# Performance work log

Hardware: AMD Instinct MI355X
Metric: run time of the kernel (lower is better)

The kernel has to match this reference:

```python
import jax, jax.numpy as jnp
import numpy as np

B, C_IN, O, K, L = 32, 64, 128, 9, 4096  # L = order*order (vec_size)


def setup_inputs() -> dict:
    key = jax.random.key(0)
    k1, k2, k3, k4 = jax.random.split(key, 4)
    x = jax.random.normal(k1, (B, C_IN, 1, L), dtype=jnp.float32)
    # precomputed irregular group-index map: each row is a permutation-like
    # index list into the vec_size axis; random in-range indices suffice for
    # a correctness baseline.
    index_matrix = jax.random.randint(k2, (K, L), 0, L, dtype=jnp.int32)
    # params (pre-normalized, matching the in-place .data normalization in
    # the torch forward, which is idempotent on already-normalized values)
    wc = jax.random.normal(k3, (O, 1, K), dtype=jnp.float32)
    weight_coeff = wc / jnp.linalg.norm(wc, axis=-1, keepdims=True)
    ev = jax.random.normal(k4, (1, L), dtype=jnp.float32)
    err_vector = ev / jnp.linalg.norm(ev)
    bias = jnp.zeros((O,), dtype=jnp.float32)
    return {"x": x, "weight_coeff": weight_coeff, "err_vector": err_vector,
            "bias": bias, "index_matrix": index_matrix}


def reference(x, weight_coeff, err_vector, bias, index_matrix):
    # normalization performed every forward call in the original module
    ev = err_vector / jnp.linalg.norm(err_vector)                      # [1, L]
    wc = weight_coeff / jnp.linalg.norm(weight_coeff, axis=-1, keepdims=True)  # [O,1,K]
    # gather neighbors via irregular index map, scale by learned vector
    adj = x[:, :, 0, index_matrix] * ev[None, None, :, :]              # [B, C_in, K, L]
    # contract over input channels i and neighborhood k
    res = jnp.einsum('ojk,bikl->bojl', wc, adj)                        # [B, O, 1, L]
    return res + bias[None, :, None, None]
```

## Files before the change

kernel.cpp:

```cpp
#include <hip/hip_runtime.h>

#define NB 32
#define NC 64
#define NO 128
#define NK 9
#define NL 4096

#define OSPLIT 4
#define OPB (NO / OSPLIT)
#define LTILE 1024
#define NLT (NL / LTILE)

typedef float vfloat4 __attribute__((ext_vector_type(4)));
typedef float vfloat2 __attribute__((ext_vector_type(2)));

__global__ __launch_bounds__(256) void colsum_kernel(
    const float* __restrict__ x, const float* __restrict__ ev,
    const float* __restrict__ wc,
    float* __restrict__ colsum, float* __restrict__ evinv,
    float* __restrict__ wcn_ws)
{
    __shared__ vfloat4 part[4][64];
    __shared__ float red[4];

    const int bid = blockIdx.x;
    const int t = threadIdx.x;

    if (bid == 0) {
        float s = 0.f;
#pragma unroll
        for (int r = 0; r < NL / 256; ++r) {
            float v = ev[r * 256 + t];
            s += v * v;
        }
#pragma unroll
        for (int off = 32; off > 0; off >>= 1) s += __shfl_down(s, off, 64);
        if ((t & 63) == 0) red[t >> 6] = s;
        if (t < NO) {
            float w[NK]; float ss = 0.f;
#pragma unroll
            for (int k = 0; k < NK; ++k) { w[k] = wc[t * NK + k]; ss += w[k] * w[k]; }
            const float inv = rsqrtf(ss);
#pragma unroll
            for (int k = 0; k < NK; ++k) wcn_ws[t * NK + k] = w[k] * inv;
        }
        __syncthreads();
        if (t == 0) evinv[0] = rsqrtf(red[0] + red[1] + red[2] + red[3]);
    }

    const int b  = bid >> 4;
    const int lt = bid & 15;
    const int col = t & 63;
    const int cg  = t >> 6;
    const int l = lt * 256 + col * 4;

    const float* xp = x + (size_t)b * NC * NL + (size_t)cg * 16 * NL + l;
    vfloat4 acc = (vfloat4){0.f, 0.f, 0.f, 0.f};
#pragma unroll
    for (int i = 0; i < 16; ++i) {
        vfloat4 v = __builtin_nontemporal_load(
            reinterpret_cast<const vfloat4*>(xp + (size_t)i * NL));
        acc += v;
    }
    part[cg][col] = acc;
    __syncthreads();
    if (t < 64) {
        vfloat4 s = part[0][t];
#pragma unroll
        for (int g = 1; g < 4; ++g) s += part[g][t];
        *reinterpret_cast<vfloat4*>(colsum + (size_t)b * NL + lt * 256 + t * 4) = s;
    }
}

__global__ __launch_bounds__(256) void gmconv_main_kernel(
    const float* __restrict__ wcn, const float* __restrict__ ev,
    const float* __restrict__ bias, const int* __restrict__ idx,
    const float* __restrict__ colsum, const float* __restrict__ evinv_p,
    float* __restrict__ out)
{
    __shared__ float csS[NL];

    const int bid = blockIdx.x;
    const int og = bid & (OSPLIT - 1);
    const int lt = (bid >> 2) & (NLT - 1);
    const int b  = bid >> 4;
    const int t  = threadIdx.x;

    const float evinv = evinv_p[0];
    const int l0 = lt * LTILE + t * 4;

    const vfloat4 e4 = *reinterpret_cast<const vfloat4*>(ev + l0);
    int4 iv[NK];
#pragma unroll
    for (int k = 0; k < NK; ++k)
        iv[k] = *reinterpret_cast<const int4*>(idx + k * NL + l0);

    const float* __restrict__ csg = colsum + (size_t)b * NL;
#pragma unroll
    for (int r = 0; r < NL / (4 * 256); ++r) {
        const int j = (r * 256 + t) * 4;
        *reinterpret_cast<vfloat4*>(&csS[j]) =
            *reinterpret_cast<const vfloat4*>(csg + j);
    }
    __syncthreads();

    const float ex = e4.x * evinv, ey = e4.y * evinv,
                ez = e4.z * evinv, ew = e4.w * evinv;

    vfloat2 g01[NK], g23[NK];
#pragma unroll
    for (int k = 0; k < NK; ++k) {
        g01[k] = (vfloat2){csS[iv[k].x] * ex, csS[iv[k].y] * ey};
        g23[k] = (vfloat2){csS[iv[k].z] * ez, csS[iv[k].w] * ew};
    }

    const int obase = og * OPB;
    float* op = out + ((size_t)b * NO + obase) * NL + l0;
#pragma unroll
    for (int o = 0; o < OPB; ++o) {
        const float* __restrict__ wr = wcn + (obase + o) * NK;
        vfloat2 a01 = (vfloat2){0.f, 0.f};
        vfloat2 a23 = (vfloat2){0.f, 0.f};
#pragma unroll
        for (int k = 0; k < NK; ++k) {
            const float w = wr[k];
            a01 += w * g01[k];
            a23 += w * g23[k];
        }
        const float bb = bias[obase + o];
        const vfloat4 r = (vfloat4){a01.x + bb, a01.y + bb, a23.x + bb, a23.y + bb};
        __builtin_nontemporal_store(r, reinterpret_cast<vfloat4*>(op));
        op += NL;
    }
}

extern "C" void kernel_launch(void* const* d_in, const int* in_sizes, int n_in,
                              void* d_out, int out_size, void* d_ws, size_t ws_size,
                              hipStream_t stream) {
    const float* x    = (const float*)d_in[0];
    const float* wc   = (const float*)d_in[1];
    const float* ev   = (const float*)d_in[2];
    const float* bias = (const float*)d_in[3];
    const int*   idx  = (const int*)d_in[4];
    float* out = (float*)d_out;

    float* wsf    = (float*)d_ws;
    float* evinv  = wsf;
    float* wcn_ws = wsf + 64;
    float* colsum = wsf + 1344;

    hipLaunchKernelGGL(colsum_kernel, dim3(NB * 16), dim3(256), 0, stream,
                       x, ev, wc, colsum, evinv, wcn_ws);
    hipLaunchKernelGGL(gmconv_main_kernel, dim3(NB * NLT * OSPLIT), dim3(256), 0,
                       stream, wcn_ws, ev, bias, idx, colsum, evinv, out);
}
```

Measured before the change: 22.92 us.

## Fuse colsum and conv kernels with per-batch atomic counter barrier

```diff
diff --git a/kernel.cpp b/kernel.cpp
--- a/kernel.cpp
+++ b/kernel.cpp
@@ -6,6 +6,8 @@
 #define NK 9
 #define NL 4096
 
+#define SLICES 16
+#define SL (NL / SLICES)
 #define OSPLIT 4
 #define OPB (NO / OSPLIT)
 #define LTILE 1024
@@ -14,99 +16,92 @@
 typedef float vfloat4 __attribute__((ext_vector_type(4)));
 typedef float vfloat2 __attribute__((ext_vector_type(2)));
 
-__global__ __launch_bounds__(256) void colsum_kernel(
-    const float* __restrict__ x, const float* __restrict__ ev,
-    const float* __restrict__ wc,
-    float* __restrict__ colsum, float* __restrict__ evinv,
-    float* __restrict__ wcn_ws)
+__global__ __launch_bounds__(256) void gmconv_fused(
+    const float* __restrict__ x, const float* __restrict__ wc,
+    const float* __restrict__ ev, const float* __restrict__ bias,
+    const int* __restrict__ idx, float* __restrict__ colsum,
+    int* __restrict__ cnt, float* __restrict__ out)
 {
     __shared__ vfloat4 part[4][64];
     __shared__ float red[4];
-
-    const int bid = blockIdx.x;
-    const int t = threadIdx.x;
-
-    if (bid == 0) {
-        float s = 0.f;
-#pragma unroll
-        for (int r = 0; r < NL / 256; ++r) {
-            float v = ev[r * 256 + t];
-            s += v * v;
-        }
-#pragma unroll
-        for (int off = 32; off > 0; off >>= 1) s += __shfl_down(s, off, 64);
-        if ((t & 63) == 0) red[t >> 6] = s;
-        if (t < NO) {
-            float w[NK]; float ss = 0.f;
-#pragma unroll
-            for (int k = 0; k < NK; ++k) { w[k] = wc[t * NK + k]; ss += w[k] * w[k]; }
-            const float inv = rsqrtf(ss);
-#pragma unroll
-            for (int k = 0; k < NK; ++k) wcn_ws[t * NK + k] = w[k] * inv;
-        }
-        __syncthreads();
-        if (t == 0) evinv[0] = rsqrtf(red[0] + red[1] + red[2] + red[3]);
-    }
-
-    const int b  = bid >> 4;
-    const int lt = bid & 15;
-    const int col = t & 63;
-    const int cg  = t >> 6;
-    const int l = lt * 256 + col * 4;
-
-    const float* xp = x + (size_t)b * NC * NL + (size_t)cg * 16 * NL + l;
-    vfloat4 acc = (vfloat4){0.f, 0.f, 0.f, 0.f};
-#pragma unroll
-    for (int i = 0; i < 16; ++i) {
-        vfloat4 v = __builtin_nontemporal_load(
-            reinterpret_cast<const vfloat4*>(xp + (size_t)i * NL));
-        acc += v;
-    }
-    part[cg][col] = acc;
-    __syncthreads();
-    if (t < 64) {
-        vfloat4 s = part[0][t];
-#pragma unroll
-        for (int g = 1; g < 4; ++g) s += part[g][t];
-        *reinterpret_cast<vfloat4*>(colsum + (size_t)b * NL + lt * 256 + t * 4) = s;
-    }
-}
-
-__global__ __launch_bounds__(256) void gmconv_main_kernel(
-    const float* __restrict__ wcn, const float* __restrict__ ev,
-    const float* __restrict__ bias, const int* __restrict__ idx,
-    const float* __restrict__ colsum, const float* __restrict__ evinv_p,
-    float* __restrict__ out)
-{
+    __shared__ float invS[OPB];
+    __shared__ vfloat2 cbS[OPB];
     __shared__ float csS[NL];
 
     const int bid = blockIdx.x;
-    const int og = bid & (OSPLIT - 1);
-    const int lt = (bid >> 2) & (NLT - 1);
+    const int j  = bid & (SLICES - 1);
     const int b  = bid >> 4;
+    const int og = j & (OSPLIT - 1);
+    const int lt = j >> 2;
     const int t  = threadIdx.x;
 
-    const float evinv = evinv_p[0];
     const int l0 = lt * LTILE + t * 4;
-
     const vfloat4 e4 = *reinterpret_cast<const vfloat4*>(ev + l0);
     int4 iv[NK];
 #pragma unroll
     for (int k = 0; k < NK; ++k)
         iv[k] = *reinterpret_cast<const int4*>(idx + k * NL + l0);
 
-    const float* __restrict__ csg = colsum + (size_t)b * NL;
+    const int col = t & 63;
+    const int cg  = t >> 6;
+    const float* xp = x + (size_t)b * NC * NL + (size_t)cg * 16 * NL
+                        + j * SL + col * 4;
+    vfloat4 xacc = (vfloat4){0.f, 0.f, 0.f, 0.f};
 #pragma unroll
-    for (int r = 0; r < NL / (4 * 256); ++r) {
-        const int j = (r * 256 + t) * 4;
-        *reinterpret_cast<vfloat4*>(&csS[j]) =
-            *reinterpret_cast<const vfloat4*>(csg + j);
+    for (int i = 0; i < 16; ++i)
+        xacc += __builtin_nontemporal_load(
+            reinterpret_cast<const vfloat4*>(xp + (size_t)i * NL));
+
+    float s = 0.f;
+#pragma unroll
+    for (int r = 0; r < 4; ++r) {
+        vfloat4 v = *reinterpret_cast<const vfloat4*>(ev + (r * 256 + t) * 4);
+        s += v.x * v.x + v.y * v.y + v.z * v.z + v.w * v.w;
+    }
+#pragma unroll
+    for (int off = 32; off > 0; off >>= 1) s += __shfl_down(s, off, 64);
+    if ((t & 63) == 0) red[t >> 6] = s;
+
+    if (t < OPB) {
+        const int o = og * OPB + t;
+        float ss = 0.f;
+#pragma unroll
+        for (int k = 0; k < NK; ++k) { const float w = wc[o * NK + k]; ss += w * w; }
+        invS[t] = rsqrtf(ss);
+    }
+    part[cg][col] = xacc;
+    __syncthreads();
+
+    const float evinv = rsqrtf(red[0] + red[1] + red[2] + red[3]);
+    if (t < OPB)
+        cbS[t] = (vfloat2){invS[t] * evinv, bias[og * OPB + t]};
+    if (t < 64) {
+        vfloat4 sl = part[0][t] + part[1][t] + part[2][t] + part[3][t];
+        *reinterpret_cast<vfloat4*>(colsum + (size_t)b * NL + j * SL + t * 4) = sl;
     }
     __syncthreads();
 
-    const float ex = e4.x * evinv, ey = e4.y * evinv,
-                ez = e4.z * evinv, ew = e4.w * evinv;
+    if (t == 0)
+        __hip_atomic_fetch_add(&cnt[b], 1, __ATOMIC_RELEASE,
+                               __HIP_MEMORY_SCOPE_AGENT);
 
+    if (t == 0) {
+        while (__hip_atomic_load(&cnt[b], __ATOMIC_ACQUIRE,
+                                 __HIP_MEMORY_SCOPE_AGENT) < SLICES)
+            __builtin_amdgcn_s_sleep(4);
+    }
+    __syncthreads();
+
+    const float* __restrict__ csg = colsum + (size_t)b * NL;
+#pragma unroll
+    for (int r = 0; r < 4; ++r) {
+        const int jj = (r * 256 + t) * 4;
+        *reinterpret_cast<vfloat4*>(&csS[jj]) =
+            *reinterpret_cast<const vfloat4*>(csg + jj);
+    }
+    __syncthreads();
+
+    const float ex = e4.x, ey = e4.y, ez = e4.z, ew = e4.w;
     vfloat2 g01[NK], g23[NK];
 #pragma unroll
     for (int k = 0; k < NK; ++k) {
@@ -118,7 +113,7 @@
     float* op = out + ((size_t)b * NO + obase) * NL + l0;
 #pragma unroll
     for (int o = 0; o < OPB; ++o) {
-        const float* __restrict__ wr = wcn + (obase + o) * NK;
+        const float* __restrict__ wr = wc + (obase + o) * NK;
         vfloat2 a01 = (vfloat2){0.f, 0.f};
         vfloat2 a23 = (vfloat2){0.f, 0.f};
 #pragma unroll
@@ -127,8 +122,9 @@
             a01 += w * g01[k];
             a23 += w * g23[k];
         }
-        const float bb = bias[obase + o];
-        const vfloat4 r = (vfloat4){a01.x + bb, a01.y + bb, a23.x + bb, a23.y + bb};
+        const vfloat2 cb = cbS[o];
+        const vfloat4 r = (vfloat4){a01.x * cb.x + cb.y, a01.y * cb.x + cb.y,
+                                    a23.x * cb.x + cb.y, a23.y * cb.x + cb.y};
         __builtin_nontemporal_store(r, reinterpret_cast<vfloat4*>(op));
         op += NL;
     }
@@ -144,13 +140,11 @@
     const int*   idx  = (const int*)d_in[4];
     float* out = (float*)d_out;
 
-    float* wsf    = (float*)d_ws;
-    float* evinv  = wsf;
-    float* wcn_ws = wsf + 64;
-    float* colsum = wsf + 1344;
+    int*   cnt    = (int*)d_ws;
+    float* colsum = (float*)d_ws + 64;
 
-    hipLaunchKernelGGL(colsum_kernel, dim3(NB * 16), dim3(256), 0, stream,
-                       x, ev, wc, colsum, evinv, wcn_ws);
-    hipLaunchKernelGGL(gmconv_main_kernel, dim3(NB * NLT * OSPLIT), dim3(256), 0,
-                       stream, wcn_ws, ev, bias, idx, colsum, evinv, out);
+    hipMemsetAsync(cnt, 0, NB * sizeof(int), stream);
+
+    hipLaunchKernelGGL(gmconv_fused, dim3(NB * SLICES), dim3(256), 0, stream,
+                       x, wc, ev, bias, idx, colsum, cnt, out);
 }
```

Result: slower. 73.53 us (+220.8%).
